# Kernel tuning notes

Measured on AMD Instinct MI355X. Metric: run time of the kernel, lower is better.

Reference implementation:

```python
import jax, jax.numpy as jnp
import numpy as np

N = 100000
E = 800000


def sage_conv(h, src, dst, W_l, W_r, b):
    # PyG SAGEConv (mean aggr): lin_l(mean_{j in N(i)} h_j) + lin_r(h_i) + bias
    deg = jax.ops.segment_sum(jnp.ones((src.shape[0],), h.dtype), dst, num_segments=N)
    agg = jax.ops.segment_sum(h[src], dst, num_segments=N)  # [N, d]
    agg = agg / jnp.maximum(deg, 1.0)[:, None]
    return agg @ W_l + h @ W_r + b


def gcn_conv(h, src, dst, W, b):
    # PyG GCNConv with added self-loops and symmetric normalization
    xw = h @ W  # [N, out]
    deg = jax.ops.segment_sum(jnp.ones((src.shape[0],), h.dtype), dst, num_segments=N) + 1.0
    dinv = jax.lax.rsqrt(deg)
    coef = dinv[src] * dinv[dst]  # [E]
    out = jax.ops.segment_sum(xw[src] * coef[:, None], dst, num_segments=N)
    out = out + xw * (1.0 / deg)[:, None]  # self-loop term: dinv[i]*dinv[i]
    return out + b


def fit_and_add(x, h):
    # initial_residual: zero-pad x along feature dim to h's width, then add
    d_in, d_out = x.shape[1], h.shape[1]
    if d_in < d_out:
        x = jnp.pad(x, ((0, 0), (0, d_out - d_in)))
    return x + h


def setup_inputs() -> dict:
    key = jax.random.key(0)
    ks = jax.random.split(key, 12)
    s = lambda d: 1.0 / np.sqrt(d)
    x = jax.random.normal(ks[0], (N, 128), jnp.float32)
    edge_index = jax.random.randint(ks[1], (2, E), 0, N, jnp.int32)
    return {
        "x": x,
        "edge_index": edge_index,
        "W1_l": jax.random.normal(ks[2], (128, 256), jnp.float32) * s(128),
        "W1_r": jax.random.normal(ks[3], (128, 256), jnp.float32) * s(128),
        "b1": jnp.zeros((256,), jnp.float32),
        "W2_l": jax.random.normal(ks[4], (256, 256), jnp.float32) * s(256),
        "W2_r": jax.random.normal(ks[5], (256, 256), jnp.float32) * s(256),
        "b2": jnp.zeros((256,), jnp.float32),
        "Wr": jax.random.normal(ks[6], (128, 256), jnp.float32) * s(128),
        "br": jnp.zeros((256,), jnp.float32),
        "Wmu": jax.random.normal(ks[7], (256, 64), jnp.float32) * s(256),
        "bmu": jnp.zeros((64,), jnp.float32),
        "Wls": jax.random.normal(ks[8], (256, 64), jnp.float32) * s(256),
        "bls": jnp.zeros((64,), jnp.float32),
    }


def reference(x, edge_index, W1_l, W1_r, b1, W2_l, W2_r, b2, Wr, br, Wmu, bmu, Wls, bls):
    src, dst = edge_index[0], edge_index[1]
    h = jax.nn.relu(sage_conv(x, src, dst, W1_l, W1_r, b1))
    h = fit_and_add(x, h)
    h = jax.nn.relu(sage_conv(h, src, dst, W2_l, W2_r, b2))
    h = h + (x @ Wr + br)
    mu = gcn_conv(h, src, dst, Wmu, bmu)
    logstd = gcn_conv(h, src, dst, Wls, bls)
    return mu, logstd
```

## Files before the change

kernel.cpp:

```cpp
#include <hip/hip_runtime.h>
#include <hip/hip_bf16.h>

#define NN 100000
#define EE 800000
#define MPAD 100096
#define MT64 1564
#define MT128 782

typedef __attribute__((ext_vector_type(4))) float f32x4;
typedef __attribute__((ext_vector_type(8))) short s16x8;

__device__ __forceinline__ float bfu(unsigned short u) {
    union { unsigned i; float f; } x; x.i = ((unsigned)u) << 16; return x.f;
}
__device__ __forceinline__ unsigned short fbf(float f) {
    union { float f; unsigned i; } x; x.f = f;
    unsigned r = x.i + (((x.i >> 16) & 1u) + 0x7fffu);
    return (unsigned short)(r >> 16);
}
__device__ __forceinline__ uint4 pack8(const float* a) {
    uint4 o;
    o.x = (unsigned)fbf(a[0]) | ((unsigned)fbf(a[1]) << 16);
    o.y = (unsigned)fbf(a[2]) | ((unsigned)fbf(a[3]) << 16);
    o.z = (unsigned)fbf(a[4]) | ((unsigned)fbf(a[5]) << 16);
    o.w = (unsigned)fbf(a[6]) | ((unsigned)fbf(a[7]) << 16);
    return o;
}
__device__ __forceinline__ void acc8(float* a, uint4 v) {
    a[0] += bfu((unsigned short)v.x); a[1] += bfu((unsigned short)(v.x >> 16));
    a[2] += bfu((unsigned short)v.y); a[3] += bfu((unsigned short)(v.y >> 16));
    a[4] += bfu((unsigned short)v.z); a[5] += bfu((unsigned short)(v.z >> 16));
    a[6] += bfu((unsigned short)v.w); a[7] += bfu((unsigned short)(v.w >> 16));
}
__device__ __forceinline__ void load_lds16(const void* g, void* l) {
    __builtin_amdgcn_global_load_lds((const __attribute__((address_space(1))) void*)g,
                                     (__attribute__((address_space(3))) void*)l, 16, 0, 0);
}


__global__ void hist_k(const int* __restrict__ ei, int* __restrict__ counts) {
    int e = blockIdx.x * 256 + threadIdx.x;
    if (e < EE) atomicAdd(&counts[ei[EE + e]], 1);
}

__global__ void scan1_k(const int* __restrict__ counts, int* __restrict__ rp, int* __restrict__ bsum) {
    __shared__ int lds[256];
    int b = blockIdx.x, t = threadIdx.x;
    int base = b * 1024 + t * 4;
    int v[4]; int s = 0;
#pragma unroll
    for (int j = 0; j < 4; ++j) { v[j] = (base + j < NN) ? counts[base + j] : 0; s += v[j]; }
    lds[t] = s; __syncthreads();
    for (int off = 1; off < 256; off <<= 1) {
        int x = (t >= off) ? lds[t - off] : 0;
        __syncthreads();
        lds[t] += x;
        __syncthreads();
    }
    int run = lds[t] - s;
    if (t == 255) bsum[b] = lds[255];
#pragma unroll
    for (int j = 0; j < 4; ++j) { if (base + j < NN) rp[base + j] = run; run += v[j]; }
}

__global__ void scan2_k(int* __restrict__ bsum, int nb) {
    int l = threadIdx.x;
    int v0 = (l < nb) ? bsum[l] : 0;
    int v1 = (64 + l < nb) ? bsum[64 + l] : 0;
    int s0 = v0, s1 = v1;
    for (int off = 1; off < 64; off <<= 1) {
        int t0 = __shfl_up(s0, off); if (l >= off) s0 += t0;
        int t1 = __shfl_up(s1, off); if (l >= off) s1 += t1;
    }
    int tot0 = __shfl(s0, 63);
    if (l < nb) bsum[l] = s0 - v0;
    if (64 + l < nb) bsum[64 + l] = tot0 + s1 - v1;
}

__global__ void scan3_k(int* __restrict__ rp, const int* __restrict__ bsum,
                        int* __restrict__ counts, float* __restrict__ dinv) {
    int i = blockIdx.x * 256 + threadIdx.x;
    if (i == 0) rp[NN] = EE;
    if (i < NN) {
        int v = rp[i] + bsum[i >> 10];
        int deg = counts[i];
        rp[i] = v;
        counts[i] = v;
        dinv[i] = rsqrtf((float)deg + 1.0f);
    }
}

__global__ void fill_k(const int* __restrict__ ei, int* __restrict__ fill, int* __restrict__ esrc) {
    int e = blockIdx.x * 256 + threadIdx.x;
    if (e < EE) {
        int d = ei[EE + e];
        int slot = atomicAdd(&fill[d], 1);
        esrc[slot] = ei[e];
    }
}


__global__ void xcvt_k(const float* __restrict__ x, __hip_bfloat16* __restrict__ A1) {
    int idx = blockIdx.x * 256 + threadIdx.x;
    if (idx < NN * 32) {
        int row = idx >> 5; int c4 = (idx & 31) * 4;
        float4 v = *(const float4*)(x + (size_t)row * 128 + c4);
        ushort4 o; o.x = fbf(v.x); o.y = fbf(v.y); o.z = fbf(v.z); o.w = fbf(v.w);
        *(ushort4*)((unsigned short*)A1 + (size_t)row * 256 + 128 + c4) = o;
    }
}

__global__ void wprep_k(const float* __restrict__ W1l, const float* __restrict__ W1r,
                        const float* __restrict__ W2l, const float* __restrict__ W2r,
                        const float* __restrict__ Wr,  const float* __restrict__ Wmu,
                        const float* __restrict__ Wls,
                        unsigned short* __restrict__ B1T, unsigned short* __restrict__ B2T,
                        unsigned short* __restrict__ B3T) {
    int idx = blockIdx.x * 256 + threadIdx.x;
    if (idx < 65536) {
        int n = idx >> 8, k = idx & 255;
        float v = (k < 128) ? W1l[k * 256 + n] : W1r[(k - 128) * 256 + n];
        B1T[idx] = fbf(v);
    } else if (idx < 229376) {
        int j = idx - 65536;
        int n = j / 640, k = j - n * 640;
        float v = (k < 256) ? W2l[k * 256 + n]
                : (k < 512) ? W2r[(k - 256) * 256 + n]
                            : Wr[(k - 512) * 256 + n];
        B2T[j] = fbf(v);
    } else if (idx < 262144) {
        int j = idx - 229376;
        int n = j >> 8, k = j & 255;
        float v = (n < 64) ? Wmu[k * 64 + n] : Wls[k * 64 + (n - 64)];
        B3T[j] = fbf(v);
    }
}


__global__ __launch_bounds__(256) void agg1_k(const int* __restrict__ rp, const int* __restrict__ esrc,
                                              __hip_bfloat16* __restrict__ A1) {
    int wid = threadIdx.x >> 6, lane = threadIdx.x & 63;
    int node = blockIdx.x * 4 + wid;
    if (node >= NN) return;
    int e0 = rp[node], e1 = rp[node + 1];
    int sg = lane >> 4, lc = lane & 15;
    const unsigned short* X = (const unsigned short*)A1;
    float a[8] = {}, b[8] = {};
    int e = e0 + sg;
    for (; e + 4 < e1; e += 8) {
        int s0 = esrc[e], s1 = esrc[e + 4];
        uint4 v0 = *(const uint4*)(X + (size_t)s0 * 256 + 128 + lc * 8);
        uint4 v1 = *(const uint4*)(X + (size_t)s1 * 256 + 128 + lc * 8);
        acc8(a, v0); acc8(b, v1);
    }
    if (e < e1) {
        uint4 v = *(const uint4*)(X + (size_t)esrc[e] * 256 + 128 + lc * 8);
        acc8(a, v);
    }
#pragma unroll
    for (int k = 0; k < 8; ++k) {
        a[k] += b[k];
        a[k] += __shfl_xor(a[k], 16);
        a[k] += __shfl_xor(a[k], 32);
    }
    int deg = e1 - e0;
    float sc = 1.0f / (float)(deg > 1 ? deg : 1);
    if (lane < 16) {
#pragma unroll
        for (int k = 0; k < 8; ++k) a[k] *= sc;
        *(uint4*)((unsigned short*)A1 + (size_t)node * 256 + lane * 8) = pack8(a);
    }
}

__global__ __launch_bounds__(256) void agg2_k(const int* __restrict__ rp, const int* __restrict__ esrc,
                                              const __hip_bfloat16* __restrict__ H1,
                                              __hip_bfloat16* __restrict__ AGG2) {
    int wid = threadIdx.x >> 6, lane = threadIdx.x & 63;
    int node = blockIdx.x * 4 + wid;
    if (node >= NN) return;
    int e0 = rp[node], e1 = rp[node + 1];
    int sg = lane >> 5, lc = lane & 31;
    const unsigned short* H = (const unsigned short*)H1;
    float a[8] = {}, b[8] = {};
    int e = e0 + sg;
    for (; e + 2 < e1; e += 4) {
        int s0 = esrc[e], s1 = esrc[e + 2];
        uint4 v0 = *(const uint4*)(H + (size_t)s0 * 256 + lc * 8);
        uint4 v1 = *(const uint4*)(H + (size_t)s1 * 256 + lc * 8);
        acc8(a, v0); acc8(b, v1);
    }
    if (e < e1) {
        uint4 v = *(const uint4*)(H + (size_t)esrc[e] * 256 + lc * 8);
        acc8(a, v);
    }
#pragma unroll
    for (int k = 0; k < 8; ++k) {
        a[k] += b[k];
        a[k] += __shfl_xor(a[k], 32);
    }
    int deg = e1 - e0;
    float sc = 1.0f / (float)(deg > 1 ? deg : 1);
    if (lane < 32) {
#pragma unroll
        for (int k = 0; k < 8; ++k) a[k] *= sc;
        *(uint4*)((unsigned short*)AGG2 + (size_t)node * 256 + lane * 8) = pack8(a);
    }
}

__global__ __launch_bounds__(256) void gcnagg_k(const int* __restrict__ rp, const int* __restrict__ esrc,
                                                const __hip_bfloat16* __restrict__ XWS,
                                                const float* __restrict__ dinv,
                                                const float* __restrict__ bmu, const float* __restrict__ bls,
                                                float* __restrict__ out) {
    int wid = threadIdx.x >> 6, lane = threadIdx.x & 63;
    int node = blockIdx.x * 4 + wid;
    if (node >= NN) return;
    int e0 = rp[node], e1 = rp[node + 1];
    int sg = lane >> 4, lc = lane & 15;
    const unsigned short* W = (const unsigned short*)XWS;
    float a[8] = {}, b[8] = {};
    if (sg == 0) {
        uint4 v = *(const uint4*)(W + (size_t)node * 128 + lc * 8);
        acc8(a, v);
    }
    int e = e0 + sg;
    for (; e + 4 < e1; e += 8) {
        int s0 = esrc[e], s1 = esrc[e + 4];
        uint4 v0 = *(const uint4*)(W + (size_t)s0 * 128 + lc * 8);
        uint4 v1 = *(const uint4*)(W + (size_t)s1 * 128 + lc * 8);
        acc8(a, v0); acc8(b, v1);
    }
    if (e < e1) {
        uint4 v = *(const uint4*)(W + (size_t)esrc[e] * 128 + lc * 8);
        acc8(a, v);
    }
#pragma unroll
    for (int k = 0; k < 8; ++k) {
        a[k] += b[k];
        a[k] += __shfl_xor(a[k], 16);
        a[k] += __shfl_xor(a[k], 32);
    }
    if (lane < 16) {
        float di = dinv[node];
        int col = lane * 8;
        float o[8];
        if (col < 64) {
#pragma unroll
            for (int k = 0; k < 8; ++k) o[k] = di * a[k] + bmu[col + k];
            *(float4*)(out + (size_t)node * 64 + col) = make_float4(o[0], o[1], o[2], o[3]);
            *(float4*)(out + (size_t)node * 64 + col + 4) = make_float4(o[4], o[5], o[6], o[7]);
        } else {
#pragma unroll
            for (int k = 0; k < 8; ++k) o[k] = di * a[k] + bls[col - 64 + k];
            *(float4*)(out + (size_t)NN * 64 + (size_t)node * 64 + (col - 64)) = make_float4(o[0], o[1], o[2], o[3]);
            *(float4*)(out + (size_t)NN * 64 + (size_t)node * 64 + (col - 60)) = make_float4(o[4], o[5], o[6], o[7]);
        }
    }
}


#define STAGE_T(SRC, LDST, STRIDE, ROWBASE, KOFF, NCH)                                              \
    _Pragma("unroll")                                                                               \
    for (int c_ = 0; c_ < NCH; ++c_) {                                                              \
        int off_ = (c_ * 256 + t) * 16;                                                             \
        int row_ = off_ >> 7;                                                                       \
        int cc_  = (off_ >> 4) & 7;                                                                 \
        int gcb_ = ((cc_ ^ (row_ & 7)) << 4);                                                       \
        int wb_ = (c_ * 256 + (t & ~63)) * 16;                                                      \
        load_lds16((const char*)(SRC) + ((size_t)((ROWBASE) + row_) * (STRIDE) + (KOFF)) * 2 + gcb_,\
                   (char*)(LDST) + wb_);                                                            \
    }

#define COMPUTE_STEP(ACC, PA, PB)                                                                  \
    _Pragma("unroll")                                                                              \
    for (int ks = 0; ks < 2; ++ks) {                                                               \
        int sc_ = (((ks << 2) + (lane >> 4)) ^ (lane & 7)) << 3;                                   \
        s16x8 afr[4], bfr[4];                                                                      \
        _Pragma("unroll")                                                                          \
        for (int i = 0; i < 4; ++i) {                                                              \
            afr[i] = *(const s16x8*)&(PA)[(wr * 64 + i * 16 + (lane & 15)) * 64 + sc_];            \
            bfr[i] = *(const s16x8*)&(PB)[(wc * 64 + i * 16 + (lane & 15)) * 64 + sc_];            \
        }                                                                                          \
        _Pragma("unroll")                                                                          \
        for (int i = 0; i < 4; ++i)                                                                \
            _Pragma("unroll")                                                                      \
            for (int j = 0; j < 4; ++j)                                                            \
                ACC[i][j] = __builtin_amdgcn_mfma_f32_16x16x32_bf16(afr[i], bfr[j], ACC[i][j], 0, 0, 0); \
    }

__global__ __launch_bounds__(256) void gemm1_k(const __hip_bfloat16* __restrict__ A1,
                                               const __hip_bfloat16* __restrict__ B1T,
                                               const float* __restrict__ b1,
                                               __hip_bfloat16* __restrict__ H1) {
    __shared__ __hip_bfloat16 lA[2][64 * 64];
    __shared__ __hip_bfloat16 lB[2][256 * 64];
    const int bm = blockIdx.x;
    const int t = threadIdx.x, lane = t & 63;
    const int wr = 0, wc = t >> 6;
    const int r0 = bm * 64;
    f32x4 acc[4][4] = {};
    STAGE_T(A1, lA[0], 256, r0, 0, 2);
    STAGE_T(B1T, lB[0], 256, 0, 0, 8);
    __syncthreads();
    int cur = 0;
    for (int kt = 0; kt < 4; ++kt) {
        if (kt < 3) {
            STAGE_T(A1, lA[cur ^ 1], 256, r0, (kt + 1) * 64, 2);
            STAGE_T(B1T, lB[cur ^ 1], 256, 0, (kt + 1) * 64, 8);
        }
        COMPUTE_STEP(acc, lA[cur], lB[cur]);
        __syncthreads();
        cur ^= 1;
    }
    const int row0 = r0, col0 = wc * 64;
    unsigned short* Hs = (unsigned short*)H1;
    const unsigned short* Xb = (const unsigned short*)A1;
#pragma unroll
    for (int i = 0; i < 4; ++i)
#pragma unroll
        for (int j = 0; j < 4; ++j) {
            int col = col0 + j * 16 + (lane & 15);
#pragma unroll
            for (int r = 0; r < 4; ++r) {
                int row = row0 + i * 16 + (lane >> 4) * 4 + r;
                float v = acc[i][j][r] + b1[col];
                v = fmaxf(v, 0.0f);
                if (col < 128) v += bfu(Xb[(size_t)row * 256 + 128 + col]);
                Hs[(size_t)row * 256 + col] = fbf(v);
            }
        }
}

__global__ __launch_bounds__(256) void gemm2_k(const __hip_bfloat16* __restrict__ AGG2,
                                               const __hip_bfloat16* __restrict__ H1,
                                               const __hip_bfloat16* __restrict__ A1,
                                               const __hip_bfloat16* __restrict__ B2T,
                                               const float* __restrict__ b2,
                                               const float* __restrict__ br,
                                               __hip_bfloat16* __restrict__ H2) {
    __shared__ __hip_bfloat16 lA[2][64 * 64];
    __shared__ __hip_bfloat16 lB[2][256 * 64];
    const int bm = blockIdx.x;
    const int t = threadIdx.x, lane = t & 63;
    const int wr = 0, wc = t >> 6;
    const int r0 = bm * 64;
    f32x4 accA[4][4] = {};
    f32x4 accB[4][4] = {};
    STAGE_T(AGG2, lA[0], 256, r0, 0, 2);
    STAGE_T(B2T, lB[0], 640, 0, 0, 8);
    __syncthreads();
    int cur = 0;
    for (int kt = 0; kt < 10; ++kt) {
        if (kt < 9) {
            int kn = kt + 1;
            const __hip_bfloat16* Ab = (kn < 4) ? AGG2 : (kn < 8 ? H1 : A1);
            int ko = (kn < 4) ? kn * 64 : (kn < 8 ? (kn - 4) * 64 : 128 + (kn - 8) * 64);
            STAGE_T(Ab, lA[cur ^ 1], 256, r0, ko, 2);
            STAGE_T(B2T, lB[cur ^ 1], 640, 0, kn * 64, 8);
        }
        if (kt < 8) {
            COMPUTE_STEP(accA, lA[cur], lB[cur]);
        } else {
            COMPUTE_STEP(accB, lA[cur], lB[cur]);
        }
        __syncthreads();
        cur ^= 1;
    }
    const int row0 = r0, col0 = wc * 64;
    unsigned short* Hs = (unsigned short*)H2;
#pragma unroll
    for (int i = 0; i < 4; ++i)
#pragma unroll
        for (int j = 0; j < 4; ++j) {
            int col = col0 + j * 16 + (lane & 15);
#pragma unroll
            for (int r = 0; r < 4; ++r) {
                int row = row0 + i * 16 + (lane >> 4) * 4 + r;
                float v = fmaxf(accA[i][j][r] + b2[col], 0.0f) + accB[i][j][r] + br[col];
                Hs[(size_t)row * 256 + col] = fbf(v);
            }
        }
}

__global__ __launch_bounds__(256) void gemm3_k(const __hip_bfloat16* __restrict__ H2,
                                               const __hip_bfloat16* __restrict__ B3T,
                                               const float* __restrict__ dinv,
                                               __hip_bfloat16* __restrict__ XWS) {
    __shared__ __hip_bfloat16 lA[2][128 * 64];
    __shared__ __hip_bfloat16 lB[2][128 * 64];
    const int bm = blockIdx.x;
    const int t = threadIdx.x, lane = t & 63, wid = t >> 6;
    const int wr = wid >> 1, wc = wid & 1;
    const int r0 = bm * 128;
    f32x4 acc[4][4] = {};
    STAGE_T(H2, lA[0], 256, r0, 0, 4);
    STAGE_T(B3T, lB[0], 256, 0, 0, 4);
    __syncthreads();
    int cur = 0;
    for (int kt = 0; kt < 4; ++kt) {
        if (kt < 3) {
            STAGE_T(H2, lA[cur ^ 1], 256, r0, (kt + 1) * 64, 4);
            STAGE_T(B3T, lB[cur ^ 1], 256, 0, (kt + 1) * 64, 4);
        }
        COMPUTE_STEP(acc, lA[cur], lB[cur]);
        __syncthreads();
        cur ^= 1;
    }
    const int row0 = r0 + wr * 64, col0 = wc * 64;
    unsigned short* Ws = (unsigned short*)XWS;
#pragma unroll
    for (int i = 0; i < 4; ++i)
#pragma unroll
        for (int j = 0; j < 4; ++j) {
            int col = col0 + j * 16 + (lane & 15);
#pragma unroll
            for (int r = 0; r < 4; ++r) {
                int row = row0 + i * 16 + (lane >> 4) * 4 + r;
                float di = (row < NN) ? dinv[row] : 0.0f;
                Ws[(size_t)row * 128 + col] = fbf(acc[i][j][r] * di);
            }
        }
}


extern "C" void kernel_launch(void* const* d_in, const int* in_sizes, int n_in,
                              void* d_out, int out_size, void* d_ws, size_t ws_size,
                              hipStream_t stream) {
    const float* x   = (const float*)d_in[0];
    const int*   ei  = (const int*)d_in[1];
    const float* W1l = (const float*)d_in[2];
    const float* W1r = (const float*)d_in[3];
    const float* b1  = (const float*)d_in[4];
    const float* W2l = (const float*)d_in[5];
    const float* W2r = (const float*)d_in[6];
    const float* b2  = (const float*)d_in[7];
    const float* Wr  = (const float*)d_in[8];
    const float* br  = (const float*)d_in[9];
    const float* Wmu = (const float*)d_in[10];
    const float* bmu = (const float*)d_in[11];
    const float* Wls = (const float*)d_in[12];
    const float* bls = (const float*)d_in[13];
    float* out = (float*)d_out;

    char* w = (char*)d_ws;
    size_t o = 0;
    int* counts = (int*)(w + o);           o += 400128;
    int* rp     = (int*)(w + o);           o += 400128;
    int* bsum   = (int*)(w + o);           o += 1024;
    int* esrc   = (int*)(w + o);           o += 3200000;
    float* dinv = (float*)(w + o);         o += 400128;
    unsigned short* B1T = (unsigned short*)(w + o); o += 131072;
    unsigned short* B2T = (unsigned short*)(w + o); o += 327680;
    unsigned short* B3T = (unsigned short*)(w + o); o += 65536;
    __hip_bfloat16* A1   = (__hip_bfloat16*)(w + o); o += (size_t)MPAD * 256 * 2;
    __hip_bfloat16* H1   = (__hip_bfloat16*)(w + o); o += (size_t)MPAD * 256 * 2;
    __hip_bfloat16* AGG2 = (__hip_bfloat16*)(w + o); o += (size_t)MPAD * 256 * 2;
    __hip_bfloat16* H2   = (__hip_bfloat16*)(w + o); o += (size_t)MPAD * 256 * 2;
    __hip_bfloat16* XWS  = AGG2;
    (void)ws_size; (void)in_sizes; (void)n_in; (void)out_size;

    hipMemsetAsync(counts, 0, NN * 4, stream);

    hist_k<<<EE / 256, 256, 0, stream>>>(ei, counts);
    scan1_k<<<98, 256, 0, stream>>>(counts, rp, bsum);
    scan2_k<<<1, 64, 0, stream>>>(bsum, 98);
    scan3_k<<<391, 256, 0, stream>>>(rp, bsum, counts, dinv);
    fill_k<<<EE / 256, 256, 0, stream>>>(ei, counts, esrc);

    xcvt_k<<<NN * 32 / 256, 256, 0, stream>>>(x, A1);
    wprep_k<<<1024, 256, 0, stream>>>(W1l, W1r, W2l, W2r, Wr, Wmu, Wls, B1T, B2T, B3T);

    agg1_k<<<NN / 4, 256, 0, stream>>>(rp, esrc, A1);
    gemm1_k<<<MT64, 256, 0, stream>>>(A1, (const __hip_bfloat16*)B1T, b1, H1);
    agg2_k<<<NN / 4, 256, 0, stream>>>(rp, esrc, H1, AGG2);
    gemm2_k<<<MT64, 256, 0, stream>>>(AGG2, H1, A1, (const __hip_bfloat16*)B2T, b2, br, H2);
    gemm3_k<<<MT128, 256, 0, stream>>>(H2, (const __hip_bfloat16*)B3T, dinv, XWS);
    gcnagg_k<<<NN / 4, 256, 0, stream>>>(rp, esrc, XWS, dinv, bmu, bls, out);
}
```

Measured before the change: 523.9 us.

## Triple-buffer LDS staging in gemm1/gemm2 with explicit vmcnt waits

Switches the two GEMM kernels from double-buffered LDS staging with two __syncthreads per tile to a three-stage ring. Tiles are prefetched two steps ahead, and each step uses a single s_barrier preceded by an explicit s_waitcnt vmcnt(10) instead of draining all outstanding loads. The goal is more global-load latency hidden behind MFMA work and fewer barriers. In exchange, LDS use grows by half (about 120KB per block), which may cut occupancy, and the hand-coded vmcnt count relies on STAGE_T issuing exactly 10 loads per tile.

```diff
diff --git a/kernel.cpp b/kernel.cpp
--- a/kernel.cpp
+++ b/kernel.cpp
@@ -288,29 +288,30 @@
                 ACC[i][j] = __builtin_amdgcn_mfma_f32_16x16x32_bf16(afr[i], bfr[j], ACC[i][j], 0, 0, 0); \
     }
 
+#define WAIT_S10() asm volatile("s_waitcnt vmcnt(10) lgkmcnt(0)" ::: "memory")
+#define WAIT_0()   asm volatile("s_waitcnt vmcnt(0) lgkmcnt(0)" ::: "memory")
+
 __global__ __launch_bounds__(256) void gemm1_k(const __hip_bfloat16* __restrict__ A1,
                                                const __hip_bfloat16* __restrict__ B1T,
                                                const float* __restrict__ b1,
                                                __hip_bfloat16* __restrict__ H1) {
-    __shared__ __hip_bfloat16 lA[2][64 * 64];
-    __shared__ __hip_bfloat16 lB[2][256 * 64];
+    __shared__ __hip_bfloat16 lA[3][64 * 64];
+    __shared__ __hip_bfloat16 lB[3][256 * 64];
     const int bm = blockIdx.x;
     const int t = threadIdx.x, lane = t & 63;
     const int wr = 0, wc = t >> 6;
     const int r0 = bm * 64;
     f32x4 acc[4][4] = {};
-    STAGE_T(A1, lA[0], 256, r0, 0, 2);
-    STAGE_T(B1T, lB[0], 256, 0, 0, 8);
-    __syncthreads();
-    int cur = 0;
+#define G1_STAGE(KN, BI)  { STAGE_T(A1, lA[BI], 256, r0, (KN) * 64, 2); \
+                            STAGE_T(B1T, lB[BI], 256, 0, (KN) * 64, 8); }
+    G1_STAGE(0, 0);
+    G1_STAGE(1, 1);
+#pragma unroll
     for (int kt = 0; kt < 4; ++kt) {
-        if (kt < 3) {
-            STAGE_T(A1, lA[cur ^ 1], 256, r0, (kt + 1) * 64, 2);
-            STAGE_T(B1T, lB[cur ^ 1], 256, 0, (kt + 1) * 64, 8);
-        }
-        COMPUTE_STEP(acc, lA[cur], lB[cur]);
-        __syncthreads();
-        cur ^= 1;
+        if (kt < 3) { WAIT_S10(); } else { WAIT_0(); }
+        __builtin_amdgcn_s_barrier();
+        if (kt + 2 < 4) { G1_STAGE(kt + 2, (kt + 2) % 3); }
+        COMPUTE_STEP(acc, lA[kt % 3], lB[kt % 3]);
     }
     const int row0 = r0, col0 = wc * 64;
     unsigned short* Hs = (unsigned short*)H1;
@@ -338,33 +339,30 @@
                                                const float* __restrict__ b2,
                                                const float* __restrict__ br,
                                                __hip_bfloat16* __restrict__ H2) {
-    __shared__ __hip_bfloat16 lA[2][64 * 64];
-    __shared__ __hip_bfloat16 lB[2][256 * 64];
+    __shared__ __hip_bfloat16 lA[3][64 * 64];
+    __shared__ __hip_bfloat16 lB[3][256 * 64];
     const int bm = blockIdx.x;
     const int t = threadIdx.x, lane = t & 63;
     const int wr = 0, wc = t >> 6;
     const int r0 = bm * 64;
     f32x4 accA[4][4] = {};
     f32x4 accB[4][4] = {};
-    STAGE_T(AGG2, lA[0], 256, r0, 0, 2);
-    STAGE_T(B2T, lB[0], 640, 0, 0, 8);
-    __syncthreads();
-    int cur = 0;
+#define G2_STAGE(KN, BI)  { const __hip_bfloat16* Ab_ = ((KN) < 4) ? AGG2 : (((KN) < 8) ? H1 : A1); \
+                            int ko_ = ((KN) < 4) ? (KN) * 64 : (((KN) < 8) ? ((KN) - 4) * 64 : 128 + ((KN) - 8) * 64); \
+                            STAGE_T(Ab_, lA[BI], 256, r0, ko_, 2); \
+                            STAGE_T(B2T, lB[BI], 640, 0, (KN) * 64, 8); }
+    G2_STAGE(0, 0);
+    G2_STAGE(1, 1);
+#pragma unroll
     for (int kt = 0; kt < 10; ++kt) {
-        if (kt < 9) {
-            int kn = kt + 1;
-            const __hip_bfloat16* Ab = (kn < 4) ? AGG2 : (kn < 8 ? H1 : A1);
-            int ko = (kn < 4) ? kn * 64 : (kn < 8 ? (kn - 4) * 64 : 128 + (kn - 8) * 64);
-            STAGE_T(Ab, lA[cur ^ 1], 256, r0, ko, 2);
-            STAGE_T(B2T, lB[cur ^ 1], 640, 0, kn * 64, 8);
-        }
+        if (kt < 9) { WAIT_S10(); } else { WAIT_0(); }
+        __builtin_amdgcn_s_barrier();
+        if (kt + 2 < 10) { G2_STAGE(kt + 2, (kt + 2) % 3); }
         if (kt < 8) {
-            COMPUTE_STEP(accA, lA[cur], lB[cur]);
+            COMPUTE_STEP(accA, lA[kt % 3], lB[kt % 3]);
         } else {
-            COMPUTE_STEP(accB, lA[cur], lB[cur]);
-        }
-        __syncthreads();
-        cur ^= 1;
+            COMPUTE_STEP(accB, lA[kt % 3], lB[kt % 3]);
+        }
     }
     const int row0 = r0, col0 = wc * 64;
     unsigned short* Hs = (unsigned short*)H2;
```

Result: slower. 568.5 us (+8.5%).

## Pre-swizzle weights into MFMA fragment order and read B directly from global

Applied to the files above, without the earlier changes.

The weight-prep kernel now writes the B matrices in per-lane MFMA fragment order, so each lane can load its B fragment as one contiguous 16-byte global read. The three GEMM kernels no longer stage B through LDS and load B fragments straight from global memory, which is expected to hit L2 because the weights are small. This cuts LDS footprint and staging traffic, which may raise occupancy. In exchange, global-load latency now sits on the MFMA path without double buffering. The k-loops are also fully unrolled.

```diff
diff --git a/kernel.cpp b/kernel.cpp
--- a/kernel.cpp
+++ b/kernel.cpp
@@ -114,25 +114,50 @@
                         const float* __restrict__ W2l, const float* __restrict__ W2r,
                         const float* __restrict__ Wr,  const float* __restrict__ Wmu,
                         const float* __restrict__ Wls,
-                        unsigned short* __restrict__ B1T, unsigned short* __restrict__ B2T,
-                        unsigned short* __restrict__ B3T) {
+                        unsigned short* __restrict__ B1F, unsigned short* __restrict__ B2F,
+                        unsigned short* __restrict__ B3F) {
     int idx = blockIdx.x * 256 + threadIdx.x;
     if (idx < 65536) {
-        int n = idx >> 8, k = idx & 255;
-        float v = (k < 128) ? W1l[k * 256 + n] : W1r[(k - 128) * 256 + n];
-        B1T[idx] = fbf(v);
+        int t = idx;
+        int e = t & 7; t >>= 3;
+        int lane = t & 63; t >>= 6;
+        int j = t & 3; t >>= 2;
+        int ks = t & 1; t >>= 1;
+        int kt = t & 3; t >>= 2;
+        int wc = t;
+        int col = wc * 64 + j * 16 + (lane & 15);
+        int k = kt * 64 + ks * 32 + (lane >> 4) * 8 + e;
+        float v = (k < 128) ? W1l[k * 256 + col] : W1r[(k - 128) * 256 + col];
+        B1F[idx] = fbf(v);
     } else if (idx < 229376) {
-        int j = idx - 65536;
-        int n = j / 640, k = j - n * 640;
-        float v = (k < 256) ? W2l[k * 256 + n]
-                : (k < 512) ? W2r[(k - 256) * 256 + n]
-                            : Wr[(k - 512) * 256 + n];
-        B2T[j] = fbf(v);
+        int t = idx - 65536;
+        int o = t;
+        int e = t & 7; t >>= 3;
+        int lane = t & 63; t >>= 6;
+        int j = t & 3; t >>= 2;
+        int ks = t & 1; t >>= 1;
+        int kt = t % 10;
+        int wc = t / 10;
+        int col = wc * 64 + j * 16 + (lane & 15);
+        int k = kt * 64 + ks * 32 + (lane >> 4) * 8 + e;
+        float v = (k < 256) ? W2l[k * 256 + col]
+                : (k < 512) ? W2r[(k - 256) * 256 + col]
+                            : Wr[(k - 512) * 256 + col];
+        B2F[o] = fbf(v);
+        (void)e;
     } else if (idx < 262144) {
-        int j = idx - 229376;
-        int n = j >> 8, k = j & 255;
-        float v = (n < 64) ? Wmu[k * 64 + n] : Wls[k * 64 + (n - 64)];
-        B3T[j] = fbf(v);
+        int t = idx - 229376;
+        int o = t;
+        int e = t & 7; t >>= 3;
+        int lane = t & 63; t >>= 6;
+        int j = t & 3; t >>= 2;
+        int ks = t & 1; t >>= 1;
+        int kt = t & 3; t >>= 2;
+        int wc = t;
+        int col = wc * 64 + j * 16 + (lane & 15);
+        int k = kt * 64 + ks * 32 + (lane >> 4) * 8 + e;
+        float v = (col < 64) ? Wmu[k * 64 + col] : Wls[k * 64 + (col - 64)];
+        B3F[o] = fbf(v);
     }
 }
 
@@ -271,16 +296,17 @@
                    (char*)(LDST) + wb_);                                                            \
     }
 
-#define COMPUTE_STEP(ACC, PA, PB)                                                                  \
+#define COMPUTE_GB(ACC, PA, BF, KT, NKT, WRBASE)                                                   \
     _Pragma("unroll")                                                                              \
     for (int ks = 0; ks < 2; ++ks) {                                                               \
         int sc_ = (((ks << 2) + (lane >> 4)) ^ (lane & 7)) << 3;                                   \
         s16x8 afr[4], bfr[4];                                                                      \
         _Pragma("unroll")                                                                          \
-        for (int i = 0; i < 4; ++i) {                                                              \
-            afr[i] = *(const s16x8*)&(PA)[(wr * 64 + i * 16 + (lane & 15)) * 64 + sc_];            \
-            bfr[i] = *(const s16x8*)&(PB)[(wc * 64 + i * 16 + (lane & 15)) * 64 + sc_];            \
-        }                                                                                          \
+        for (int j = 0; j < 4; ++j)                                                                \
+            bfr[j] = *(const s16x8*)((BF) + (size_t)((((((wc) * (NKT) + (KT)) * 2 + ks) * 4 + j) * 64 + lane) << 3)); \
+        _Pragma("unroll")                                                                          \
+        for (int i = 0; i < 4; ++i)                                                                \
+            afr[i] = *(const s16x8*)&(PA)[((WRBASE) + i * 16 + (lane & 15)) * 64 + sc_];           \
         _Pragma("unroll")                                                                          \
         for (int i = 0; i < 4; ++i)                                                                \
             _Pragma("unroll")                                                                      \
@@ -289,26 +315,22 @@
     }
 
 __global__ __launch_bounds__(256) void gemm1_k(const __hip_bfloat16* __restrict__ A1,
-                                               const __hip_bfloat16* __restrict__ B1T,
+                                               const unsigned short* __restrict__ B1F,
                                                const float* __restrict__ b1,
                                                __hip_bfloat16* __restrict__ H1) {
     __shared__ __hip_bfloat16 lA[2][64 * 64];
-    __shared__ __hip_bfloat16 lB[2][256 * 64];
     const int bm = blockIdx.x;
     const int t = threadIdx.x, lane = t & 63;
-    const int wr = 0, wc = t >> 6;
+    const int wc = t >> 6;
     const int r0 = bm * 64;
     f32x4 acc[4][4] = {};
     STAGE_T(A1, lA[0], 256, r0, 0, 2);
-    STAGE_T(B1T, lB[0], 256, 0, 0, 8);
     __syncthreads();
     int cur = 0;
+#pragma unroll
     for (int kt = 0; kt < 4; ++kt) {
-        if (kt < 3) {
-            STAGE_T(A1, lA[cur ^ 1], 256, r0, (kt + 1) * 64, 2);
-            STAGE_T(B1T, lB[cur ^ 1], 256, 0, (kt + 1) * 64, 8);
-        }
-        COMPUTE_STEP(acc, lA[cur], lB[cur]);
+        if (kt < 3) { STAGE_T(A1, lA[cur ^ 1], 256, r0, (kt + 1) * 64, 2); }
+        COMPUTE_GB(acc, lA[cur], B1F, kt, 4, 0);
         __syncthreads();
         cur ^= 1;
     }
@@ -334,34 +356,32 @@
 __global__ __launch_bounds__(256) void gemm2_k(const __hip_bfloat16* __restrict__ AGG2,
                                                const __hip_bfloat16* __restrict__ H1,
                                                const __hip_bfloat16* __restrict__ A1,
-                                               const __hip_bfloat16* __restrict__ B2T,
+                                               const unsigned short* __restrict__ B2F,
                                                const float* __restrict__ b2,
                                                const float* __restrict__ br,
                                                __hip_bfloat16* __restrict__ H2) {
     __shared__ __hip_bfloat16 lA[2][64 * 64];
-    __shared__ __hip_bfloat16 lB[2][256 * 64];
     const int bm = blockIdx.x;
     const int t = threadIdx.x, lane = t & 63;
-    const int wr = 0, wc = t >> 6;
+    const int wc = t >> 6;
     const int r0 = bm * 64;
     f32x4 accA[4][4] = {};
     f32x4 accB[4][4] = {};
     STAGE_T(AGG2, lA[0], 256, r0, 0, 2);
-    STAGE_T(B2T, lB[0], 640, 0, 0, 8);
     __syncthreads();
     int cur = 0;
+#pragma unroll
     for (int kt = 0; kt < 10; ++kt) {
         if (kt < 9) {
             int kn = kt + 1;
             const __hip_bfloat16* Ab = (kn < 4) ? AGG2 : (kn < 8 ? H1 : A1);
             int ko = (kn < 4) ? kn * 64 : (kn < 8 ? (kn - 4) * 64 : 128 + (kn - 8) * 64);
             STAGE_T(Ab, lA[cur ^ 1], 256, r0, ko, 2);
-            STAGE_T(B2T, lB[cur ^ 1], 640, 0, kn * 64, 8);
         }
         if (kt < 8) {
-            COMPUTE_STEP(accA, lA[cur], lB[cur]);
+            COMPUTE_GB(accA, lA[cur], B2F, kt, 10, 0);
         } else {
-            COMPUTE_STEP(accB, lA[cur], lB[cur]);
+            COMPUTE_GB(accB, lA[cur], B2F, kt, 10, 0);
         }
         __syncthreads();
         cur ^= 1;
@@ -383,26 +403,22 @@
 }
 
 __global__ __launch_bounds__(256) void gemm3_k(const __hip_bfloat16* __restrict__ H2,
-                                               const __hip_bfloat16* __restrict__ B3T,
+                                               const unsigned short* __restrict__ B3F,
                                                const float* __restrict__ dinv,
                                                __hip_bfloat16* __restrict__ XWS) {
     __shared__ __hip_bfloat16 lA[2][128 * 64];
-    __shared__ __hip_bfloat16 lB[2][128 * 64];
     const int bm = blockIdx.x;
     const int t = threadIdx.x, lane = t & 63, wid = t >> 6;
     const int wr = wid >> 1, wc = wid & 1;
     const int r0 = bm * 128;
     f32x4 acc[4][4] = {};
     STAGE_T(H2, lA[0], 256, r0, 0, 4);
-    STAGE_T(B3T, lB[0], 256, 0, 0, 4);
     __syncthreads();
     int cur = 0;
+#pragma unroll
     for (int kt = 0; kt < 4; ++kt) {
-        if (kt < 3) {
-            STAGE_T(H2, lA[cur ^ 1], 256, r0, (kt + 1) * 64, 4);
-            STAGE_T(B3T, lB[cur ^ 1], 256, 0, (kt + 1) * 64, 4);
-        }
-        COMPUTE_STEP(acc, lA[cur], lB[cur]);
+        if (kt < 3) { STAGE_T(H2, lA[cur ^ 1], 256, r0, (kt + 1) * 64, 4); }
+        COMPUTE_GB(acc, lA[cur], B3F, kt, 4, wr * 64);
         __syncthreads();
         cur ^= 1;
     }
@@ -449,9 +465,9 @@
     int* bsum   = (int*)(w + o);           o += 1024;
     int* esrc   = (int*)(w + o);           o += 3200000;
     float* dinv = (float*)(w + o);         o += 400128;
-    unsigned short* B1T = (unsigned short*)(w + o); o += 131072;
-    unsigned short* B2T = (unsigned short*)(w + o); o += 327680;
-    unsigned short* B3T = (unsigned short*)(w + o); o += 65536;
+    unsigned short* B1F = (unsigned short*)(w + o); o += 131072;
+    unsigned short* B2F = (unsigned short*)(w + o); o += 327680;
+    unsigned short* B3F = (unsigned short*)(w + o); o += 65536;
     __hip_bfloat16* A1   = (__hip_bfloat16*)(w + o); o += (size_t)MPAD * 256 * 2;
     __hip_bfloat16* H1   = (__hip_bfloat16*)(w + o); o += (size_t)MPAD * 256 * 2;
     __hip_bfloat16* AGG2 = (__hip_bfloat16*)(w + o); o += (size_t)MPAD * 256 * 2;
@@ -468,12 +484,12 @@
     fill_k<<<EE / 256, 256, 0, stream>>>(ei, counts, esrc);
 
     xcvt_k<<<NN * 32 / 256, 256, 0, stream>>>(x, A1);
-    wprep_k<<<1024, 256, 0, stream>>>(W1l, W1r, W2l, W2r, Wr, Wmu, Wls, B1T, B2T, B3T);
+    wprep_k<<<1024, 256, 0, stream>>>(W1l, W1r, W2l, W2r, Wr, Wmu, Wls, B1F, B2F, B3F);
 
     agg1_k<<<NN / 4, 256, 0, stream>>>(rp, esrc, A1);
-    gemm1_k<<<MT64, 256, 0, stream>>>(A1, (const __hip_bfloat16*)B1T, b1, H1);
+    gemm1_k<<<MT64, 256, 0, stream>>>(A1, B1F, b1, H1);
     agg2_k<<<NN / 4, 256, 0, stream>>>(rp, esrc, H1, AGG2);
-    gemm2_k<<<MT64, 256, 0, stream>>>(AGG2, H1, A1, (const __hip_bfloat16*)B2T, b2, br, H2);
-    gemm3_k<<<MT128, 256, 0, stream>>>(H2, (const __hip_bfloat16*)B3T, dinv, XWS);
+    gemm2_k<<<MT64, 256, 0, stream>>>(AGG2, H1, A1, B2F, b2, br, H2);
+    gemm3_k<<<MT128, 256, 0, stream>>>(H2, B3F, dinv, XWS);
     gcnagg_k<<<NN / 4, 256, 0, stream>>>(rp, esrc, XWS, dinv, bmu, bls, out);
 }
```

Measured after the change: 505.9 us. 3.4% less time.
